# Kernel optimization log

Hardware: AMD Instinct MI355X
Metric: run time of the kernel (lower is better)

The kernel has to match this reference:

```python
import jax, jax.numpy as jnp
import numpy as np

N_NODES = 100000
N_EDGES = 400000  # per edge type
N_ETYPES = 3
N_LAYERS = 3      # 1 + (n_layers-1) + 1 with n_layers=2
D = 64


def setup_inputs() -> dict:
    key = jax.random.key(0)
    k1, k2, k3, k4, k5 = jax.random.split(key, 5)
    feat = jax.random.normal(k1, (N_NODES, D), dtype=jnp.float32)
    # SAGEConv weights per (layer, etype): fc_self, fc_neigh, bias
    W_self = jax.random.normal(k2, (N_LAYERS, N_ETYPES, D, D), dtype=jnp.float32) * 0.05
    W_neigh = jax.random.normal(k3, (N_LAYERS, N_ETYPES, D, D), dtype=jnp.float32) * 0.05
    b = jnp.zeros((N_LAYERS, N_ETYPES, D), dtype=jnp.float32)
    src = jax.random.randint(k4, (N_ETYPES, N_EDGES), 0, N_NODES, dtype=jnp.int32)
    dst = jax.random.randint(k5, (N_ETYPES, N_EDGES), 0, N_NODES, dtype=jnp.int32)
    return {"feat": feat, "W_self": W_self, "W_neigh": W_neigh, "b": b,
            "src": src, "dst": dst}


def reference(feat, W_self, W_neigh, b, src, dst):
    # Heterogeneous SAGEConv (mean aggregator) + cross-relation sum, 3 layers.
    N = feat.shape[0]
    L, T = W_self.shape[0], W_self.shape[1]
    E = src.shape[1]
    ones = jnp.ones((E,), dtype=feat.dtype)
    h = feat
    for l in range(L):
        apply_act = l < L - 1  # last layer has no activation
        out = jnp.zeros((N, W_self.shape[-1]), dtype=feat.dtype)
        for t in range(T):  # small fixed set of relation types
            msgs = jnp.take(h, src[t], axis=0)                    # [E, d] gather
            agg = jax.ops.segment_sum(msgs, dst[t], num_segments=N)   # [N, d]
            deg = jax.ops.segment_sum(ones, dst[t], num_segments=N)   # [N]
            mean = agg / jnp.maximum(deg, 1.0)[:, None]           # zero-deg -> 0
            r = h @ W_self[l, t] + mean @ W_neigh[l, t] + b[l, t]
            if apply_act:
                r = jax.nn.relu(r)
            out = out + r  # HeteroGraphConv aggregate='sum'
        h = out
    return h
```

## Files before the change

kernel.cpp:

```cpp
#include <hip/hip_runtime.h>
#include <hip/hip_bf16.h>

#define NN 100000
#define NE 400000
#define NT 3
#define NL 3
#define DD 64
#define M_TOT (NT * NN)
#define RPB 2048
#define NBKT ((M_TOT + RPB - 1) / RPB)
#define P3CAP 32
#define P3GRID 256
#define PCAP 13312
#define SUBR 512
#define NSUB 4
#define COLCAP_SUB 2304
#define OVF_CAP 500000


typedef __attribute__((ext_vector_type(8))) short bf16x8;
typedef __attribute__((ext_vector_type(4))) float f32x4;

static __device__ __forceinline__ unsigned short f2b(float f) {
    __hip_bfloat16 b = __float2bfloat16(f);
    return *reinterpret_cast<unsigned short*>(&b);
}
static __device__ __forceinline__ float b2f(unsigned short u) {
    __hip_bfloat16 b = *reinterpret_cast<__hip_bfloat16*>(&u);
    return __bfloat162float(b);
}

__global__ void init_kernel(int* __restrict__ gcur, int* __restrict__ ocnt) {
    int i = threadIdx.x;
    if (i < NBKT) gcur[i] = i * PCAP;
    if (i == 0) ocnt[0] = 0;
}

__global__ __launch_bounds__(256) void pair_scatter(
    const int* __restrict__ src, const int* __restrict__ dst,
    int* __restrict__ gcur, unsigned* __restrict__ pairs,
    uint2* __restrict__ ovf, int* __restrict__ ocnt) {
    __shared__ unsigned buf[NBKT][P3CAP];
    __shared__ int fill[NBKT];
    for (int i = threadIdx.x; i < NBKT; i += 256) fill[i] = 0;
    __syncthreads();
    const int total = NT * NE;
    int per = (total + gridDim.x - 1) / gridDim.x;
    int beg = blockIdx.x * per;
    int fin = beg + per; if (fin > total) fin = total;
    for (int bse = beg; bse < fin; bse += 256) {
        int e = bse + threadIdx.x;
        if (e < fin) {
            int t = e / NE;
            int row = t * NN + dst[e];
            int bk = row >> 11;
            unsigned pr = ((unsigned)(row & 2047) << 17) | (unsigned)src[e];
            int pos = atomicAdd(&fill[bk], 1);
            if (pos < P3CAP) buf[bk][pos] = pr;
            else {
                int o = atomicAdd(ocnt, 1);
                if (o < OVF_CAP) ovf[o] = make_uint2((unsigned)src[e], (unsigned)row);
            }
        }
        __syncthreads();
        for (int bk = threadIdx.x; bk < NBKT; bk += 256) {
            int n = fill[bk]; if (n > P3CAP) n = P3CAP;
            int g = n >> 4;
            if (g) {
                int gb = atomicAdd(&gcur[bk], g * 16);
#pragma unroll
                for (int q = 0; q < 4; ++q)
                    *(int4*)&pairs[gb + q * 4] = *(const int4*)&buf[bk][q * 4];
                if (g == 2)
#pragma unroll
                    for (int q = 0; q < 4; ++q)
                        *(int4*)&pairs[gb + 16 + q * 4] =
                            *(const int4*)&buf[bk][16 + q * 4];
                int rem = n - g * 16;
                for (int k = 0; k < rem; ++k) buf[bk][k] = buf[bk][g * 16 + k];
                fill[bk] = rem;
            } else fill[bk] = n;
        }
        __syncthreads();
    }
    for (int bk = threadIdx.x; bk < NBKT; bk += 256) {
        int n = fill[bk]; if (n > P3CAP) n = P3CAP;
        if (n) {
            int m = (n + 15) & ~15;
            for (int k = n; k < m; ++k) buf[bk][k] = 0xFFFFFFFFu;
            int gb = atomicAdd(&gcur[bk], m);
            for (int grp = 0; grp < m >> 4; ++grp)
#pragma unroll
                for (int q = 0; q < 4; ++q)
                    *(int4*)&pairs[gb + grp * 16 + q * 4] =
                        *(const int4*)&buf[bk][grp * 16 + q * 4];
        }
    }
}

__global__ __launch_bounds__(256) void bucket_csr(
    const int* __restrict__ gcur, const unsigned* __restrict__ pairs,
    const uint2* __restrict__ ovf, const int* __restrict__ ocnt,
    int* __restrict__ rs, int* __restrict__ rse, int* __restrict__ col) {
    __shared__ int cnt_s[SUBR];
    __shared__ int cur_s[SUBR];
    __shared__ int part[256];
    const int blk = blockIdx.x;
    const int bk = blk >> 2, sub = blk & 3;
    const int row0 = bk * RPB + sub * SUBR;
    const int rl0 = sub * SUBR;
    const int nrows = (M_TOT - row0 < SUBR) ? (M_TOT - row0) : SUBR;
    for (int i = threadIdx.x; i < SUBR; i += 256) cnt_s[i] = 0;
    __syncthreads();
    const int pb = bk * PCAP, pe = gcur[bk];
    for (int p = pb + threadIdx.x; p < pe; p += 256) {
        unsigned pr = pairs[p];
        if ((pr & 0x1FFFFu) < NN) {
            int rl = (int)(pr >> 17) - rl0;
            if (rl >= 0 && rl < nrows) atomicAdd(&cnt_s[rl], 1);
        }
    }
    int no = ocnt[0]; if (no > OVF_CAP) no = OVF_CAP;
    for (int o = threadIdx.x; o < no; o += 256) {
        int rl = (int)ovf[o].y - row0;
        if (rl >= 0 && rl < nrows) atomicAdd(&cnt_s[rl], 1);
    }
    __syncthreads();
    int t0 = threadIdx.x * 2, sum = 0;
    int exl[2];
#pragma unroll
    for (int k = 0; k < 2; ++k) { exl[k] = sum; sum += cnt_s[t0 + k]; }
    part[threadIdx.x] = sum;
    __syncthreads();
    for (int o = 1; o < 256; o <<= 1) {
        int v = (threadIdx.x >= o) ? part[threadIdx.x - o] : 0;
        __syncthreads();
        part[threadIdx.x] += v;
        __syncthreads();
    }
    int off = part[threadIdx.x] - sum + blk * COLCAP_SUB;
#pragma unroll
    for (int k = 0; k < 2; ++k) {
        int idx = t0 + k;
        int ex = exl[k] + off;
        cur_s[idx] = ex;
        if (idx < nrows) { rs[row0 + idx] = ex; rse[row0 + idx] = ex + cnt_s[idx]; }
    }
    __syncthreads();
    for (int p = pb + threadIdx.x; p < pe; p += 256) {
        unsigned pr = pairs[p];
        unsigned s = pr & 0x1FFFFu;
        if (s < NN) {
            int rl = (int)(pr >> 17) - rl0;
            if (rl >= 0 && rl < nrows) {
                int pos = atomicAdd(&cur_s[rl], 1);
                col[pos] = (int)s;
            }
        }
    }
    for (int o = threadIdx.x; o < no; o += 256) {
        int rl = (int)ovf[o].y - row0;
        if (rl >= 0 && rl < nrows) {
            int pos = atomicAdd(&cur_s[rl], 1);
            col[pos] = (int)ovf[o].x;
        }
    }
}

__global__ __launch_bounds__(256) void wtrans_kernel(
    const float* __restrict__ Ws, const float* __restrict__ Wn,
    unsigned short* __restrict__ Wt) {
    int lt = blockIdx.x;
    for (int p = threadIdx.x; p < DD * 2 * DD; p += 256) {
        int j = p >> 7, k = p & 127;
        float v = (k < DD) ? Ws[(size_t)lt * DD * DD + k * DD + j]
                           : Wn[(size_t)lt * DD * DD + (k - DD) * DD + j];
        Wt[(size_t)lt * 8192 + j * 128 + k] = f2b(v);
    }
}

template <int HBF>
__global__ __launch_bounds__(256) void gather_kernel(
    const void* __restrict__ hv, const int* __restrict__ rs,
    const int* __restrict__ rse, const int* __restrict__ col,
    unsigned short* __restrict__ meanb) {
    const int lane = threadIdx.x & 63;
    const int g = lane >> 3;
    const int fc = lane & 7;
    const int i = (blockIdx.x * 4 + (threadIdx.x >> 6)) * 8 + g;
    const bool live = i < M_TOT;
    const int start = live ? rs[i] : 0;
    const int end   = live ? rse[i] : 0;
    const int deg = end - start;
    int md = deg;
    { int t = __shfl_xor(md, 8);  md = md > t ? md : t; }
    { int t = __shfl_xor(md, 16); md = md > t ? md : t; }
    { int t = __shfl_xor(md, 32); md = md > t ? md : t; }
    float acc[8];
#pragma unroll
    for (int j = 0; j < 8; ++j) acc[j] = 0.f;
    const unsigned short* hb = (const unsigned short*)hv;
    const float* hf = (const float*)hv;
    for (int base = 0; base < md; base += 8) {
        int e = start + base + fc;
        int cl = col[(e < end) ? e : 0];

#define GSTEP(K)                                                               \
        {                                                                      \
            int idx = __builtin_amdgcn_ds_swizzle(cl, ((K) << 5) | 24);        \
            bool v = (base + (K)) < deg;                                       \
            float mk = v ? 1.f : 0.f;                                          \
            int ix = v ? idx : 0;                                              \
            if (HBF) {                                                         \
                int4 rv = *(const int4*)&hb[(size_t)ix * DD + fc * 8];         \
                const unsigned* wp = (const unsigned*)&rv;                     \
                _Pragma("unroll")                                              \
                for (int j = 0; j < 4; ++j) {                                  \
                    unsigned w = wp[j];                                        \
                    float lo = __uint_as_float(w << 16);                       \
                    float hi = __uint_as_float(w & 0xffff0000u);               \
                    acc[2 * j]     = fmaf(lo, mk, acc[2 * j]);                 \
                    acc[2 * j + 1] = fmaf(hi, mk, acc[2 * j + 1]);             \
                }                                                              \
            } else {                                                           \
                float4 a = *(const float4*)&hf[(size_t)ix * DD + fc * 8];      \
                float4 b = *(const float4*)&hf[(size_t)ix * DD + fc * 8 + 4];  \
                acc[0] = fmaf(a.x, mk, acc[0]);                                \
                acc[1] = fmaf(a.y, mk, acc[1]);                                \
                acc[2] = fmaf(a.z, mk, acc[2]);                                \
                acc[3] = fmaf(a.w, mk, acc[3]);                                \
                acc[4] = fmaf(b.x, mk, acc[4]);                                \
                acc[5] = fmaf(b.y, mk, acc[5]);                                \
                acc[6] = fmaf(b.z, mk, acc[6]);                                \
                acc[7] = fmaf(b.w, mk, acc[7]);                                \
            }                                                                  \
        }
        GSTEP(0) GSTEP(1) GSTEP(2) GSTEP(3)
        GSTEP(4) GSTEP(5) GSTEP(6) GSTEP(7)
#undef GSTEP
    }
    float sc = (deg > 0) ? 1.f / (float)deg : 0.f;
    unsigned ow[4];
#pragma unroll
    for (int j = 0; j < 4; ++j) {
        unsigned lo = f2b(acc[2 * j] * sc);
        unsigned hi = f2b(acc[2 * j + 1] * sc);
        ow[j] = lo | (hi << 16);
    }
    if (live)
        *(int4*)&meanb[(size_t)i * DD + fc * 8] = *(const int4*)ow;
}

template <int HBF, int OBF>
__global__ __launch_bounds__(256) void layer_gemm(
    const void* __restrict__ hv, const unsigned short* __restrict__ meanb,
    const unsigned short* __restrict__ Wt, const float* __restrict__ bias,
    void* __restrict__ outv, int relu) {
    __shared__ __align__(16) short A_s[64 * 136];
    __shared__ __align__(16) short B_s[64 * 136];

    const int tx = threadIdx.x;
    const int n0 = blockIdx.x * 64;
    const int lane = tx & 63, w = tx >> 6;
    const int q = lane >> 4, m16 = lane & 15;
    const int rr = tx >> 4;
    const int k0 = (tx & 15) * 4;
    const int bj = tx >> 2;
    const int bk = (tx & 3) * 32;

#pragma unroll
    for (int qq = 0; qq < 4; ++qq) {
        int r = rr + 16 * qq;
        int n = n0 + r;
        ushort4 hb4 = make_ushort4(0, 0, 0, 0);
        if (n < NN) {
            if (HBF) {
                hb4 = *(const ushort4*)&((const unsigned short*)hv)[(size_t)n * DD + k0];
            } else {
                float4 hf = *(const float4*)&((const float*)hv)[(size_t)n * DD + k0];
                hb4 = make_ushort4(f2b(hf.x), f2b(hf.y), f2b(hf.z), f2b(hf.w));
            }
        }
        *(ushort4*)&A_s[r * 136 + k0] = hb4;
    }

    float acc_sum[4][4];
#pragma unroll
    for (int c = 0; c < 4; ++c)
#pragma unroll
        for (int r = 0; r < 4; ++r) acc_sum[c][r] = 0.f;

    for (int t = 0; t < NT; ++t) {
#pragma unroll
        for (int qq = 0; qq < 4; ++qq) {
            int r = rr + 16 * qq;
            int n = n0 + r;
            ushort4 mv = make_ushort4(0, 0, 0, 0);
            if (n < NN)
                mv = *(const ushort4*)&meanb[((size_t)t * NN + n) * DD + k0];
            *(ushort4*)&A_s[r * 136 + 64 + k0] = mv;
        }
        {
            const unsigned short* wt = Wt + (size_t)t * 8192 + bj * 128 + bk;
#pragma unroll
            for (int u = 0; u < 4; ++u)
                *(int4*)&B_s[bj * 136 + bk + u * 8] = *(const int4*)&wt[u * 8];
        }
        __syncthreads();

        f32x4 acc[4];
#pragma unroll
        for (int c = 0; c < 4; ++c) acc[c] = (f32x4){0.f, 0.f, 0.f, 0.f};
#pragma unroll
        for (int kt = 0; kt < 4; ++kt) {
            bf16x8 a = *(const bf16x8*)&A_s[(16 * w + m16) * 136 + kt * 32 + q * 8];
#pragma unroll
            for (int c = 0; c < 4; ++c) {
                bf16x8 b = *(const bf16x8*)&B_s[(c * 16 + m16) * 136 + kt * 32 + q * 8];
                acc[c] = __builtin_amdgcn_mfma_f32_16x16x32_bf16(a, b, acc[c], 0, 0, 0);
            }
        }

#pragma unroll
        for (int c = 0; c < 4; ++c) {
            float bv = bias[t * DD + c * 16 + m16];
#pragma unroll
            for (int r = 0; r < 4; ++r) {
                float v = acc[c][r] + bv;
                if (relu) v = fmaxf(v, 0.f);
                acc_sum[c][r] += v;
            }
        }
        __syncthreads();
    }

#pragma unroll
    for (int c = 0; c < 4; ++c)
#pragma unroll
        for (int r = 0; r < 4; ++r) {
            int n = n0 + 16 * w + q * 4 + r;
            if (n >= NN) continue;
            size_t idx = (size_t)n * DD + c * 16 + m16;
            if (OBF)
                ((unsigned short*)outv)[idx] = f2b(acc_sum[c][r]);
            else
                ((float*)outv)[idx] = acc_sum[c][r];
        }
}

extern "C" void kernel_launch(void* const* d_in, const int* in_sizes, int n_in,
                              void* d_out, int out_size, void* d_ws, size_t ws_size,
                              hipStream_t stream) {
    const float* feat    = (const float*)d_in[0];
    const float* W_self  = (const float*)d_in[1];
    const float* W_neigh = (const float*)d_in[2];
    const float* bias    = (const float*)d_in[3];
    const int* src = (const int*)d_in[4];
    const int* dst = (const int*)d_in[5];

    char* ws = (char*)d_ws;
    int* gcur  = (int*)(ws + 0);
    int* ocnt  = (int*)(ws + 1024);
    int* rs    = (int*)(ws + 8192);
    int* rse   = (int*)(ws + 1208320);
    int* col   = (int*)(ws + 2408448);
    unsigned short* Wt    = (unsigned short*)(ws + 7827584);
    unsigned short* X2    = (unsigned short*)(ws + 7975040);
    unsigned short* meanb = (unsigned short*)(ws + 20775040);
    unsigned*       pairs = (unsigned*)(ws + 20775040);
    uint2*          ovf   = (uint2*)(ws + 20775040 + 8388608);

    init_kernel<<<1, 256, 0, stream>>>(gcur, ocnt);
    pair_scatter<<<P3GRID, 256, 0, stream>>>(src, dst, gcur, pairs, ovf, ocnt);
    bucket_csr<<<NBKT * NSUB, 256, 0, stream>>>(gcur, pairs, ovf, ocnt,
                                                rs, rse, col);
    wtrans_kernel<<<NL * NT, 256, 0, stream>>>(W_self, W_neigh, Wt);

    unsigned short* X1 = (unsigned short*)d_out;
    const int ggrid = (M_TOT + 31) / 32;
    const int mgrid = (NN + 63) / 64;

    gather_kernel<0><<<ggrid, 256, 0, stream>>>(feat, rs, rse, col, meanb);
    layer_gemm<0, 1><<<mgrid, 256, 0, stream>>>(
        feat, meanb, Wt + 0 * NT * 8192, bias + 0 * NT * DD, X1, 1);
    gather_kernel<1><<<ggrid, 256, 0, stream>>>(X1, rs, rse, col, meanb);
    layer_gemm<1, 1><<<mgrid, 256, 0, stream>>>(
        X1, meanb, Wt + 1 * NT * 8192, bias + 1 * NT * DD, X2, 1);
    gather_kernel<1><<<ggrid, 256, 0, stream>>>(X2, rs, rse, col, meanb);
    layer_gemm<1, 0><<<mgrid, 256, 0, stream>>>(
        X2, meanb, Wt + 2 * NT * 8192, bias + 2 * NT * DD, d_out, 0);
}
```

Baseline: 318.1 us.

## Load GEMM operands directly into registers and use per-row gather loop bounds

The layer GEMM no longer stages node features, mean aggregates and weights through shared memory with barriers. Each lane now loads its MFMA A fragments straight from global memory and reads B fragments from the small weight matrix, which should stay in cache. The gather kernel drops the cross-lane max-degree reduction and loops per row over its own degree, padding out-of-range edges with the row's start index. The swizzle-based index broadcast assumes all lanes in a group stay converged, which is a risk when rows in the same 8-lane group have different degrees.

```diff
diff --git a/kernel.cpp b/kernel.cpp
--- a/kernel.cpp
+++ b/kernel.cpp
@@ -192,18 +192,14 @@
     const int start = live ? rs[i] : 0;
     const int end   = live ? rse[i] : 0;
     const int deg = end - start;
-    int md = deg;
-    { int t = __shfl_xor(md, 8);  md = md > t ? md : t; }
-    { int t = __shfl_xor(md, 16); md = md > t ? md : t; }
-    { int t = __shfl_xor(md, 32); md = md > t ? md : t; }
     float acc[8];
 #pragma unroll
     for (int j = 0; j < 8; ++j) acc[j] = 0.f;
     const unsigned short* hb = (const unsigned short*)hv;
     const float* hf = (const float*)hv;
-    for (int base = 0; base < md; base += 8) {
+    for (int base = 0; base < deg; base += 8) {
         int e = start + base + fc;
-        int cl = col[(e < end) ? e : 0];
+        int cl = col[(e < end) ? e : start];
 
 #define GSTEP(K)                                                               \
         {                                                                      \
@@ -256,32 +252,39 @@
     const void* __restrict__ hv, const unsigned short* __restrict__ meanb,
     const unsigned short* __restrict__ Wt, const float* __restrict__ bias,
     void* __restrict__ outv, int relu) {
-    __shared__ __align__(16) short A_s[64 * 136];
-    __shared__ __align__(16) short B_s[64 * 136];
-
     const int tx = threadIdx.x;
     const int n0 = blockIdx.x * 64;
     const int lane = tx & 63, w = tx >> 6;
     const int q = lane >> 4, m16 = lane & 15;
-    const int rr = tx >> 4;
-    const int k0 = (tx & 15) * 4;
-    const int bj = tx >> 2;
-    const int bk = (tx & 3) * 32;
-
-#pragma unroll
-    for (int qq = 0; qq < 4; ++qq) {
-        int r = rr + 16 * qq;
-        int n = n0 + r;
-        ushort4 hb4 = make_ushort4(0, 0, 0, 0);
-        if (n < NN) {
-            if (HBF) {
-                hb4 = *(const ushort4*)&((const unsigned short*)hv)[(size_t)n * DD + k0];
-            } else {
-                float4 hf = *(const float4*)&((const float*)hv)[(size_t)n * DD + k0];
-                hb4 = make_ushort4(f2b(hf.x), f2b(hf.y), f2b(hf.z), f2b(hf.w));
-            }
-        }
-        *(ushort4*)&A_s[r * 136 + k0] = hb4;
+    const int row = n0 + 16 * w + m16;
+    const bool rlive = row < NN;
+
+    bf16x8 zero8;
+#pragma unroll
+    for (int j = 0; j < 8; ++j) zero8[j] = 0;
+
+    bf16x8 aself[2];
+    if (rlive) {
+        if (HBF) {
+            const unsigned short* hr = (const unsigned short*)hv + (size_t)row * DD;
+            aself[0] = *(const bf16x8*)&hr[q * 8];
+            aself[1] = *(const bf16x8*)&hr[32 + q * 8];
+        } else {
+            const float* hr = (const float*)hv + (size_t)row * DD;
+#pragma unroll
+            for (int h = 0; h < 2; ++h) {
+                float4 f0 = *(const float4*)&hr[h * 32 + q * 8];
+                float4 f1 = *(const float4*)&hr[h * 32 + q * 8 + 4];
+                bf16x8 t;
+                t[0] = (short)f2b(f0.x); t[1] = (short)f2b(f0.y);
+                t[2] = (short)f2b(f0.z); t[3] = (short)f2b(f0.w);
+                t[4] = (short)f2b(f1.x); t[5] = (short)f2b(f1.y);
+                t[6] = (short)f2b(f1.z); t[7] = (short)f2b(f1.w);
+                aself[h] = t;
+            }
+        }
+    } else {
+        aself[0] = zero8; aself[1] = zero8;
     }
 
     float acc_sum[4][4];
@@ -291,32 +294,25 @@
         for (int r = 0; r < 4; ++r) acc_sum[c][r] = 0.f;
 
     for (int t = 0; t < NT; ++t) {
-#pragma unroll
-        for (int qq = 0; qq < 4; ++qq) {
-            int r = rr + 16 * qq;
-            int n = n0 + r;
-            ushort4 mv = make_ushort4(0, 0, 0, 0);
-            if (n < NN)
-                mv = *(const ushort4*)&meanb[((size_t)t * NN + n) * DD + k0];
-            *(ushort4*)&A_s[r * 136 + 64 + k0] = mv;
-        }
-        {
-            const unsigned short* wt = Wt + (size_t)t * 8192 + bj * 128 + bk;
-#pragma unroll
-            for (int u = 0; u < 4; ++u)
-                *(int4*)&B_s[bj * 136 + bk + u * 8] = *(const int4*)&wt[u * 8];
-        }
-        __syncthreads();
+        bf16x8 am[2];
+        if (rlive) {
+            const unsigned short* mr = meanb + ((size_t)t * NN + row) * DD;
+            am[0] = *(const bf16x8*)&mr[q * 8];
+            am[1] = *(const bf16x8*)&mr[32 + q * 8];
+        } else {
+            am[0] = zero8; am[1] = zero8;
+        }
+        const unsigned short* wt = Wt + (size_t)t * 8192;
 
         f32x4 acc[4];
 #pragma unroll
         for (int c = 0; c < 4; ++c) acc[c] = (f32x4){0.f, 0.f, 0.f, 0.f};
 #pragma unroll
         for (int kt = 0; kt < 4; ++kt) {
-            bf16x8 a = *(const bf16x8*)&A_s[(16 * w + m16) * 136 + kt * 32 + q * 8];
+            bf16x8 a = (kt < 2) ? aself[kt] : am[kt - 2];
 #pragma unroll
             for (int c = 0; c < 4; ++c) {
-                bf16x8 b = *(const bf16x8*)&B_s[(c * 16 + m16) * 136 + kt * 32 + q * 8];
+                bf16x8 b = *(const bf16x8*)&wt[(c * 16 + m16) * 128 + kt * 32 + q * 8];
                 acc[c] = __builtin_amdgcn_mfma_f32_16x16x32_bf16(a, b, acc[c], 0, 0, 0);
             }
         }
@@ -331,7 +327,6 @@
                 acc_sum[c][r] += v;
             }
         }
-        __syncthreads();
     }
 
 #pragma unroll
```

Result: slower. 394.5 us (+24.0%).

## Prefetch next relation's mean and weights into registers; drop wave-max degree loop

Applied to the files above, without the earlier changes.

In the layer GEMM, the mean rows and weight tile for the next relation type are loaded into registers while the current relation's MFMAs run, so global-load latency overlaps compute instead of sitting in front of each barrier. The relation loop is also fully unrolled. In the gather kernel, each 8-lane group now loops to its own degree rather than the max over the wave, dropping three shuffles. Groups can now diverge within a wave, and the prefetch raises register pressure.

```diff
diff --git a/kernel.cpp b/kernel.cpp
--- a/kernel.cpp
+++ b/kernel.cpp
@@ -192,18 +192,14 @@
     const int start = live ? rs[i] : 0;
     const int end   = live ? rse[i] : 0;
     const int deg = end - start;
-    int md = deg;
-    { int t = __shfl_xor(md, 8);  md = md > t ? md : t; }
-    { int t = __shfl_xor(md, 16); md = md > t ? md : t; }
-    { int t = __shfl_xor(md, 32); md = md > t ? md : t; }
     float acc[8];
 #pragma unroll
     for (int j = 0; j < 8; ++j) acc[j] = 0.f;
     const unsigned short* hb = (const unsigned short*)hv;
     const float* hf = (const float*)hv;
-    for (int base = 0; base < md; base += 8) {
+    for (int base = 0; base < deg; base += 8) {
         int e = start + base + fc;
-        int cl = col[(e < end) ? e : 0];
+        int cl = col[(e < end) ? e : start];
 
 #define GSTEP(K)                                                               \
         {                                                                      \
@@ -256,7 +252,7 @@
     const void* __restrict__ hv, const unsigned short* __restrict__ meanb,
     const unsigned short* __restrict__ Wt, const float* __restrict__ bias,
     void* __restrict__ outv, int relu) {
-    __shared__ __align__(16) short A_s[64 * 136];
+    __shared__ __align__(16) short AM_s[64 * 136];
     __shared__ __align__(16) short B_s[64 * 136];
 
     const int tx = threadIdx.x;
@@ -281,7 +277,22 @@
                 hb4 = make_ushort4(f2b(hf.x), f2b(hf.y), f2b(hf.z), f2b(hf.w));
             }
         }
-        *(ushort4*)&A_s[r * 136 + k0] = hb4;
+        *(ushort4*)&AM_s[r * 136 + k0] = hb4;
+    }
+
+    ushort4 mreg[4];
+    int4 breg[4];
+#pragma unroll
+    for (int qq = 0; qq < 4; ++qq) {
+        int n = n0 + rr + 16 * qq;
+        mreg[qq] = make_ushort4(0, 0, 0, 0);
+        if (n < NN)
+            mreg[qq] = *(const ushort4*)&meanb[((size_t)0 * NN + n) * DD + k0];
+    }
+    {
+        const unsigned short* wt = Wt + bj * 128 + bk;
+#pragma unroll
+        for (int u = 0; u < 4; ++u) breg[u] = *(const int4*)&wt[u * 8];
     }
 
     float acc_sum[4][4];
@@ -290,21 +301,28 @@
 #pragma unroll
         for (int r = 0; r < 4; ++r) acc_sum[c][r] = 0.f;
 
+    const int arow = (16 * w + m16) * 136;
+
+#pragma unroll
     for (int t = 0; t < NT; ++t) {
 #pragma unroll
-        for (int qq = 0; qq < 4; ++qq) {
-            int r = rr + 16 * qq;
-            int n = n0 + r;
-            ushort4 mv = make_ushort4(0, 0, 0, 0);
-            if (n < NN)
-                mv = *(const ushort4*)&meanb[((size_t)t * NN + n) * DD + k0];
-            *(ushort4*)&A_s[r * 136 + 64 + k0] = mv;
-        }
-        {
-            const unsigned short* wt = Wt + (size_t)t * 8192 + bj * 128 + bk;
-#pragma unroll
-            for (int u = 0; u < 4; ++u)
-                *(int4*)&B_s[bj * 136 + bk + u * 8] = *(const int4*)&wt[u * 8];
+        for (int qq = 0; qq < 4; ++qq)
+            *(ushort4*)&AM_s[(rr + 16 * qq) * 136 + 64 + k0] = mreg[qq];
+#pragma unroll
+        for (int u = 0; u < 4; ++u)
+            *(int4*)&B_s[bj * 136 + bk + u * 8] = breg[u];
+
+        if (t < NT - 1) {
+#pragma unroll
+            for (int qq = 0; qq < 4; ++qq) {
+                int n = n0 + rr + 16 * qq;
+                mreg[qq] = make_ushort4(0, 0, 0, 0);
+                if (n < NN)
+                    mreg[qq] = *(const ushort4*)&meanb[((size_t)(t + 1) * NN + n) * DD + k0];
+            }
+            const unsigned short* wt = Wt + (size_t)(t + 1) * 8192 + bj * 128 + bk;
+#pragma unroll
+            for (int u = 0; u < 4; ++u) breg[u] = *(const int4*)&wt[u * 8];
         }
         __syncthreads();
 
@@ -313,7 +331,7 @@
         for (int c = 0; c < 4; ++c) acc[c] = (f32x4){0.f, 0.f, 0.f, 0.f};
 #pragma unroll
         for (int kt = 0; kt < 4; ++kt) {
-            bf16x8 a = *(const bf16x8*)&A_s[(16 * w + m16) * 136 + kt * 32 + q * 8];
+            bf16x8 a = *(const bf16x8*)&AM_s[arow + kt * 32 + q * 8];
 #pragma unroll
             for (int c = 0; c < 4; ++c) {
                 bf16x8 b = *(const bf16x8*)&B_s[(c * 16 + m16) * 136 + kt * 32 + q * 8];
```

Measured after the change: 341.7 us. 1.07x slower.

## Build CSR with one 1024-thread block per bucket; loop gather on per-row degree

Applied to the files above, without the earlier changes.

bucket_csr now runs one 1024-thread block per 2048-row bucket instead of four 256-thread sub-blocks. Previously each sub-block re-read the whole bucket's pair list and discarded rows outside its slice, so pairs were read four times; now they are read once and the per-row range checks go away. The gather kernel drops the wave-wide max-degree shuffle reduction and loops on each row's own degree. Since lanes in a wave still run in lockstep, that second change mostly saves the shuffles. The trade-off is fewer, larger CSR blocks with a longer shared-memory scan.

```diff
diff --git a/kernel.cpp b/kernel.cpp
--- a/kernel.cpp
+++ b/kernel.cpp
@@ -12,9 +12,8 @@
 #define P3CAP 32
 #define P3GRID 256
 #define PCAP 13312
-#define SUBR 512
-#define NSUB 4
-#define COLCAP_SUB 2304
+#define CSR_THREADS 1024
+#define COLCAP_BKT 9216
 #define OVF_CAP 500000
 
 
@@ -98,30 +97,26 @@
     }
 }
 
-__global__ __launch_bounds__(256) void bucket_csr(
+__global__ __launch_bounds__(CSR_THREADS) void bucket_csr(
     const int* __restrict__ gcur, const unsigned* __restrict__ pairs,
     const uint2* __restrict__ ovf, const int* __restrict__ ocnt,
     int* __restrict__ rs, int* __restrict__ rse, int* __restrict__ col) {
-    __shared__ int cnt_s[SUBR];
-    __shared__ int cur_s[SUBR];
-    __shared__ int part[256];
-    const int blk = blockIdx.x;
-    const int bk = blk >> 2, sub = blk & 3;
-    const int row0 = bk * RPB + sub * SUBR;
-    const int rl0 = sub * SUBR;
-    const int nrows = (M_TOT - row0 < SUBR) ? (M_TOT - row0) : SUBR;
-    for (int i = threadIdx.x; i < SUBR; i += 256) cnt_s[i] = 0;
+    __shared__ int cnt_s[RPB];
+    __shared__ int cur_s[RPB];
+    __shared__ int part[CSR_THREADS];
+    const int bk = blockIdx.x;
+    const int row0 = bk * RPB;
+    const int nrows = (M_TOT - row0 < RPB) ? (M_TOT - row0) : RPB;
+    for (int i = threadIdx.x; i < RPB; i += CSR_THREADS) cnt_s[i] = 0;
     __syncthreads();
     const int pb = bk * PCAP, pe = gcur[bk];
-    for (int p = pb + threadIdx.x; p < pe; p += 256) {
+    for (int p = pb + threadIdx.x; p < pe; p += CSR_THREADS) {
         unsigned pr = pairs[p];
-        if ((pr & 0x1FFFFu) < NN) {
-            int rl = (int)(pr >> 17) - rl0;
-            if (rl >= 0 && rl < nrows) atomicAdd(&cnt_s[rl], 1);
-        }
+        if ((pr & 0x1FFFFu) < NN)
+            atomicAdd(&cnt_s[pr >> 17], 1);
     }
     int no = ocnt[0]; if (no > OVF_CAP) no = OVF_CAP;
-    for (int o = threadIdx.x; o < no; o += 256) {
+    for (int o = threadIdx.x; o < no; o += CSR_THREADS) {
         int rl = (int)ovf[o].y - row0;
         if (rl >= 0 && rl < nrows) atomicAdd(&cnt_s[rl], 1);
     }
@@ -132,13 +127,13 @@
     for (int k = 0; k < 2; ++k) { exl[k] = sum; sum += cnt_s[t0 + k]; }
     part[threadIdx.x] = sum;
     __syncthreads();
-    for (int o = 1; o < 256; o <<= 1) {
+    for (int o = 1; o < CSR_THREADS; o <<= 1) {
         int v = (threadIdx.x >= o) ? part[threadIdx.x - o] : 0;
         __syncthreads();
         part[threadIdx.x] += v;
         __syncthreads();
     }
-    int off = part[threadIdx.x] - sum + blk * COLCAP_SUB;
+    int off = part[threadIdx.x] - sum + bk * COLCAP_BKT;
 #pragma unroll
     for (int k = 0; k < 2; ++k) {
         int idx = t0 + k;
@@ -147,18 +142,15 @@
         if (idx < nrows) { rs[row0 + idx] = ex; rse[row0 + idx] = ex + cnt_s[idx]; }
     }
     __syncthreads();
-    for (int p = pb + threadIdx.x; p < pe; p += 256) {
+    for (int p = pb + threadIdx.x; p < pe; p += CSR_THREADS) {
         unsigned pr = pairs[p];
         unsigned s = pr & 0x1FFFFu;
         if (s < NN) {
-            int rl = (int)(pr >> 17) - rl0;
-            if (rl >= 0 && rl < nrows) {
-                int pos = atomicAdd(&cur_s[rl], 1);
-                col[pos] = (int)s;
-            }
-        }
-    }
-    for (int o = threadIdx.x; o < no; o += 256) {
+            int pos = atomicAdd(&cur_s[pr >> 17], 1);
+            col[pos] = (int)s;
+        }
+    }
+    for (int o = threadIdx.x; o < no; o += CSR_THREADS) {
         int rl = (int)ovf[o].y - row0;
         if (rl >= 0 && rl < nrows) {
             int pos = atomicAdd(&cur_s[rl], 1);
@@ -192,18 +184,14 @@
     const int start = live ? rs[i] : 0;
     const int end   = live ? rse[i] : 0;
     const int deg = end - start;
-    int md = deg;
-    { int t = __shfl_xor(md, 8);  md = md > t ? md : t; }
-    { int t = __shfl_xor(md, 16); md = md > t ? md : t; }
-    { int t = __shfl_xor(md, 32); md = md > t ? md : t; }
     float acc[8];
 #pragma unroll
     for (int j = 0; j < 8; ++j) acc[j] = 0.f;
     const unsigned short* hb = (const unsigned short*)hv;
     const float* hf = (const float*)hv;
-    for (int base = 0; base < md; base += 8) {
+    for (int base = 0; base < deg; base += 8) {
         int e = start + base + fc;
-        int cl = col[(e < end) ? e : 0];
+        int cl = col[(e < end) ? e : start];
 
 #define GSTEP(K)                                                               \
         {                                                                      \
@@ -372,8 +360,8 @@
 
     init_kernel<<<1, 256, 0, stream>>>(gcur, ocnt);
     pair_scatter<<<P3GRID, 256, 0, stream>>>(src, dst, gcur, pairs, ovf, ocnt);
-    bucket_csr<<<NBKT * NSUB, 256, 0, stream>>>(gcur, pairs, ovf, ocnt,
-                                                rs, rse, col);
+    bucket_csr<<<NBKT, CSR_THREADS, 0, stream>>>(gcur, pairs, ovf, ocnt,
+                                                 rs, rse, col);
     wtrans_kernel<<<NL * NT, 256, 0, stream>>>(W_self, W_neigh, Wt);
 
     unsigned short* X1 = (unsigned short*)d_out;
```

Result: faster. 302.9 us (-4.8%).
